# Optimization experiments

Hardware: AMD Instinct MI355X
Metric: run time of the kernel (lower is better)

The kernel has to match this reference:

```python
import jax, jax.numpy as jnp
import numpy as np

# dims
B, S, D, H, DH, M, L, V, BS, NR = 4, 2048, 512, 8, 64, 2048, 6, 32000, 64, 3
NB = S // BS  # 32 blocks


def _block_plan(nb, seed):
    """BigBird block connectivity: 2 global + 3 window + NR random blocks per query block.
    Returns idx [nb, K] int32 and validity mask [nb, K] bool (dedup + edge handling)."""
    rng = np.random.RandomState(seed)
    K = 5 + NR
    idx = np.zeros((nb, K), np.int32)
    msk = np.zeros((nb, K), bool)
    for i in range(nb):
        fixed = {0, nb - 1} | {j for j in (i - 1, i, i + 1) if 0 <= j < nb}
        rest = [j for j in range(nb) if j not in fixed]
        rnd = rng.choice(rest, size=min(NR, len(rest)), replace=False) if rest else []
        sel = sorted(fixed | set(int(r) for r in rnd))
        idx[i, :len(sel)] = sel
        msk[i, :len(sel)] = True
    return jnp.asarray(idx), jnp.asarray(msk)


def _posemb():
    pos = np.arange(S, dtype=np.float32)[:, None]
    div = np.exp(np.arange(0, D, 2, dtype=np.float32) * (-np.log(10000.0) / D))
    pe = np.zeros((S, D), np.float32)
    pe[:, 0::2] = np.sin(pos * div)
    pe[:, 1::2] = np.cos(pos * div)
    return jnp.asarray(pe)


def _ln(x, scale, bias):
    m = jnp.mean(x, axis=-1, keepdims=True)
    v = jnp.mean(jnp.square(x - m), axis=-1, keepdims=True)
    return (x - m) * jax.lax.rsqrt(v + 1e-6) * scale + bias


def _bigbird_attn(x, key_mask, wq, wk, wv, wo, idx, bmask):
    # x: [B,S,D]; idx/bmask: [NB,K]
    q = jnp.einsum('bsd,dhe->bshe', x, wq).reshape(B, NB, BS, H, DH)
    k = jnp.einsum('bsd,dhe->bshe', x, wk).reshape(B, NB, BS, H, DH)
    v = jnp.einsum('bsd,dhe->bshe', x, wv).reshape(B, NB, BS, H, DH)
    kg = k[:, idx]  # [B,NB,K,BS,H,DH] gathered key blocks
    vg = v[:, idx]
    scores = jnp.einsum('bnqhe,bnkche->bhnqkc', q, kg) / jnp.sqrt(jnp.float32(DH))
    kmb = key_mask.reshape(B, NB, BS)[:, idx]          # [B,NB,K,BS]
    m = kmb & bmask[None, :, :, None]                   # [B,NB,K,BS]
    scores = jnp.where(m[:, None, :, None, :, :], scores, jnp.float32(-1e9))
    Kc = idx.shape[1]
    attn = jax.nn.softmax(scores.reshape(B, H, NB, BS, Kc * BS), axis=-1)
    attn = attn.reshape(B, H, NB, BS, Kc, BS)
    out = jnp.einsum('bhnqkc,bnkche->bnqhe', attn, vg).reshape(B, S, H, DH)
    return jnp.einsum('bshe,hed->bsd', out, wo)


def setup_inputs() -> dict:
    key = jax.random.key(0)
    ks = jax.random.split(key, 12)
    n = jax.random.normal
    inp = {
        'tokens': jax.random.randint(ks[0], (B, S), 0, V, dtype=jnp.int32),
        'embed': n(ks[1], (V, D), dtype=jnp.float32),
        'ln1_s': jnp.ones((L, D), jnp.float32), 'ln1_b': jnp.zeros((L, D), jnp.float32),
        'wq': n(ks[2], (L, D, H, DH), dtype=jnp.float32) * 0.02,
        'wk': n(ks[3], (L, D, H, DH), dtype=jnp.float32) * 0.02,
        'wv': n(ks[4], (L, D, H, DH), dtype=jnp.float32) * 0.02,
        'wo': n(ks[5], (L, H, DH, D), dtype=jnp.float32) * 0.02,
        'ln2_s': jnp.ones((L, D), jnp.float32), 'ln2_b': jnp.zeros((L, D), jnp.float32),
        'w1': n(ks[6], (L, D, M), dtype=jnp.float32) * 0.02, 'b1': jnp.zeros((L, M), jnp.float32),
        'w2': n(ks[7], (L, M, D), dtype=jnp.float32) * 0.02, 'b2': jnp.zeros((L, D), jnp.float32),
        'lnf_s': jnp.ones((D,), jnp.float32), 'lnf_b': jnp.zeros((D,), jnp.float32),
    }
    return inp


def reference(tokens, embed, ln1_s, ln1_b, wq, wk, wv, wo, ln2_s, ln2_b, w1, b1, w2, b2, lnf_s, lnf_b):
    key_mask = tokens > 0                      # src padding mask
    x = embed[tokens] + _posemb()[None]        # [B,S,D]
    plans = [_block_plan(NB, l) for l in range(L)]  # connectivity_seed = layer index
    for l in range(L):
        idx, bm = plans[l]
        h = _ln(x, ln1_s[l], ln1_b[l])
        x = x + _bigbird_attn(h, key_mask, wq[l], wk[l], wv[l], wo[l], idx, bm)
        y = _ln(x, ln2_s[l], ln2_b[l])
        y = jax.nn.gelu(jnp.einsum('bsd,dm->bsm', y, w1[l]) + b1[l])
        y = jnp.einsum('bsm,md->bsd', y, w2[l]) + b2[l]
        x = x + y
    return _ln(x, lnf_s, lnf_b)
```

## Files before the change

### kernel.cpp

```cpp
#include <hip/hip_runtime.h>

using u32 = unsigned int;
using u16 = unsigned short;

#define B_   4
#define S_   2048
#define D_   512
#define H_   8
#define DH_  64
#define FF_  2048
#define L_   6
#define NB_  32
#define KC_  8

typedef __attribute__((ext_vector_type(8))) __bf16 bf16x8;
typedef __attribute__((ext_vector_type(4))) float  f32x4;

struct Plan { unsigned char idx[NB_][KC_]; unsigned char cnt[NB_]; };

#define QSCALE 0.18033688011112042f

__device__ __forceinline__ u16 f2b(float f) {
  union { __bf16 b; u16 u; } x;
  x.b = (__bf16)f;
  return x.u;
}

__device__ __forceinline__ float gelu_f(float x) {
  float y2 = 1.5957691216f * x + 0.0713548163f * x * x * x;
  return x / (1.0f + __expf(-y2));
}

typedef const __attribute__((address_space(1))) u32* gas_t;
typedef __attribute__((address_space(3))) u32* las_t;
__device__ __forceinline__ void glds16(const u16* g, u16* l) {
  __builtin_amdgcn_global_load_lds((gas_t)g, (las_t)l, 16, 0, 0);
}

__global__ __launch_bounds__(256)
void transpose_conv(const float* __restrict__ in, u16* __restrict__ out, int R, int C,
                    size_t lstride, int rowoff) {
  __shared__ float tile[32][33];
  const int l = blockIdx.z;
  const float* src = in + (size_t)l * R * C;
  u16* dst = out + (size_t)l * lstride;
  const int c0 = blockIdx.x * 32, r0 = blockIdx.y * 32;
  const int tx = threadIdx.x, ty = threadIdx.y;
#pragma unroll
  for (int i = 0; i < 4; i++)
    tile[ty + i * 8][tx] = src[(size_t)(r0 + ty + i * 8) * C + c0 + tx];
  __syncthreads();
#pragma unroll
  for (int i = 0; i < 4; i++)
    dst[(size_t)(rowoff + c0 + ty + i * 8) * R + r0 + tx] = f2b(tile[tx][ty + i * 8]);
}

__global__ __launch_bounds__(128)
void embed_kernel(const int* __restrict__ tokens, const float* __restrict__ emb,
                  float* __restrict__ x) {
  const int row = blockIdx.x;
  const int s = row & (S_ - 1);
  const int t = threadIdx.x;
  const int tok = tokens[row];
  float4 v = ((const float4*)(emb + (size_t)tok * D_))[t];
  float va[4] = {v.x, v.y, v.z, v.w};
  const float cc = -2.0f * logf(10000.0f) / (float)D_;
  const float pos = (float)s;
#pragma unroll
  for (int j = 0; j < 4; j++) {
    int d = t * 4 + j;
    int i = d >> 1;
    float dv = expf(cc * (float)i);
    float ang = pos * dv;
    va[j] += (d & 1) ? cosf(ang) : sinf(ang);
  }
  ((float4*)x)[(size_t)row * (D_ / 4) + t] = make_float4(va[0], va[1], va[2], va[3]);
}

template <bool BF16OUT>
__global__ __launch_bounds__(128)
void ln_kernel(const float* __restrict__ x, const float* __restrict__ sc,
               const float* __restrict__ bi, void* __restrict__ outp) {
  const int row = blockIdx.x;
  const int t = threadIdx.x;
  float4 v = ((const float4*)(x + (size_t)row * D_))[t];
  float va[4] = {v.x, v.y, v.z, v.w};
  float s = va[0] + va[1] + va[2] + va[3];
  float sq = va[0] * va[0] + va[1] * va[1] + va[2] * va[2] + va[3] * va[3];
#pragma unroll
  for (int d = 1; d < 64; d <<= 1) {
    s  += __shfl_xor(s, d);
    sq += __shfl_xor(sq, d);
  }
  __shared__ float red[4];
  const int wv = t >> 6, lane = t & 63;
  if (lane == 0) { red[wv * 2] = s; red[wv * 2 + 1] = sq; }
  __syncthreads();
  const float ts  = red[0] + red[2];
  const float tsq = red[1] + red[3];
  const float mean = ts * (1.0f / (float)D_);
  const float inv  = rsqrtf(tsq * (1.0f / (float)D_) - mean * mean + 1e-6f);
  const int d0 = t * 4;
  float o[4];
#pragma unroll
  for (int j = 0; j < 4; j++)
    o[j] = (va[j] - mean) * inv * sc[d0 + j] + bi[d0 + j];
  if (BF16OUT) {
    ushort4 u;
    u.x = f2b(o[0]); u.y = f2b(o[1]); u.z = f2b(o[2]); u.w = f2b(o[3]);
    ((ushort4*)outp)[(size_t)row * (D_ / 4) + t] = u;
  } else {
    ((float4*)outp)[(size_t)row * (D_ / 4) + t] = make_float4(o[0], o[1], o[2], o[3]);
  }
}

template <int MODE, bool VSPLIT, int T>
__global__ __launch_bounds__(T * 2)
void gemm_pipe(const u16* __restrict__ A, const u16* __restrict__ BT,
               int Kk, int ostride,
               float* __restrict__ outf, u16* __restrict__ outb,
               const float* __restrict__ bias, const float* __restrict__ resid,
               u16* __restrict__ vtout) {
  constexpr int MI = T / 32;
  constexpr int NW = T / 64;
  __shared__ u16 As[2][T * 64];
  __shared__ u16 Bs[2][T * 64];
  const int tid = threadIdx.x;
  const int wave = tid >> 6, lane = tid & 63;
  const int row0 = blockIdx.x * T, col0 = blockIdx.y * T;
  const int wr = wave / NW, wc = wave % NW;
  const int l15 = lane & 15, l4 = lane >> 4;

  const u16* asrc[4];
  const u16* bsrc[4];
  int cdst[4];
#pragma unroll
  for (int i = 0; i < 4; i++) {
    int chunk = wave * 256 + i * 64 + lane;
    int r = chunk >> 3, s = chunk & 7;
    int ss = (s ^ (r & 7)) << 3;
    asrc[i] = A  + (size_t)(row0 + r) * Kk + ss;
    bsrc[i] = BT + (size_t)(col0 + r) * Kk + ss;
    cdst[i] = (wave * 256 + i * 64) * 8;
  }

  int aoff[MI], boff[4];
#pragma unroll
  for (int m = 0; m < MI; m++) aoff[m] = (wr * (MI * 16) + m * 16 + l15) * 64;
#pragma unroll
  for (int n = 0; n < 4; n++) boff[n] = (wc * 64 + n * 16 + l15) * 64;
  const int sk0 = ((l4)     ^ (l15 & 7)) << 3;
  const int sk1 = ((4 + l4) ^ (l15 & 7)) << 3;

  f32x4 acc[MI][4] = {};
  const int nk = Kk >> 6;

  auto stage = [&](int buf, int kt) {
    const int ko = kt << 6;
#pragma unroll
    for (int i = 0; i < 4; i++) glds16(asrc[i] + ko, &As[buf][cdst[i]]);
#pragma unroll
    for (int i = 0; i < 4; i++) glds16(bsrc[i] + ko, &Bs[buf][cdst[i]]);
  };

  stage(0, 0);
  stage(1, 1);

  for (int kt = 0; kt < nk; ++kt) {
    const int cur = kt & 1;
    if (kt + 1 < nk) { asm volatile("s_waitcnt vmcnt(8)" ::: "memory"); }
    else             { asm volatile("s_waitcnt vmcnt(0)" ::: "memory"); }
    __builtin_amdgcn_s_barrier();
    __builtin_amdgcn_sched_barrier(0);

    bf16x8 af0[MI], bf0[4];
#pragma unroll
    for (int m = 0; m < MI; m++) af0[m] = *(const bf16x8*)&As[cur][aoff[m] + sk0];
#pragma unroll
    for (int n = 0; n < 4; n++) bf0[n] = *(const bf16x8*)&Bs[cur][boff[n] + sk0];
#pragma unroll
    for (int m = 0; m < MI; m++)
#pragma unroll
      for (int n = 0; n < 4; n++)
        acc[m][n] = __builtin_amdgcn_mfma_f32_16x16x32_bf16(af0[m], bf0[n], acc[m][n], 0, 0, 0);

    bf16x8 af1[MI], bf1[4];
#pragma unroll
    for (int m = 0; m < MI; m++) af1[m] = *(const bf16x8*)&As[cur][aoff[m] + sk1];
#pragma unroll
    for (int n = 0; n < 4; n++) bf1[n] = *(const bf16x8*)&Bs[cur][boff[n] + sk1];
    asm volatile("s_waitcnt lgkmcnt(0)" ::: "memory");
    __builtin_amdgcn_sched_barrier(0);
    __builtin_amdgcn_s_barrier();
    __builtin_amdgcn_sched_barrier(0);
    if (kt + 2 < nk) stage(cur, kt + 2);

    __builtin_amdgcn_s_setprio(1);
#pragma unroll
    for (int m = 0; m < MI; m++)
#pragma unroll
      for (int n = 0; n < 4; n++)
        acc[m][n] = __builtin_amdgcn_mfma_f32_16x16x32_bf16(af1[m], bf1[n], acc[m][n], 0, 0, 0);
    __builtin_amdgcn_s_setprio(0);
  }

#pragma unroll
  for (int m = 0; m < MI; m++) {
#pragma unroll
    for (int n = 0; n < 4; n++) {
      const int c = col0 + wc * 64 + n * 16 + l15;
      const int rb = row0 + wr * (MI * 16) + m * 16 + l4 * 4;
      if (VSPLIT && c >= 1024) {
        u16 pk[4];
#pragma unroll
        for (int j = 0; j < 4; j++) pk[j] = f2b(acc[m][n][j]);
        *(uint2*)(vtout + (size_t)(c - 1024) * (B_ * S_) + rb) = *(const uint2*)pk;
      } else {
#pragma unroll
        for (int j = 0; j < 4; j++) {
          const size_t o = (size_t)(rb + j) * ostride + c;
          float v = acc[m][n][j];
          if (MODE == 0) {
            if (VSPLIT && c < 512) v *= QSCALE;
            outb[o] = f2b(v);
          } else if (MODE == 1) {
            outf[o] = v + resid[o];
          } else if (MODE == 2) {
            outb[o] = f2b(gelu_f(v + bias[c]));
          } else {
            outf[o] = v + bias[c] + resid[o];
          }
        }
      }
    }
  }
}

__global__ __launch_bounds__(256, 4)
void attn_mfma(const u16* __restrict__ qkv, const u16* __restrict__ vTg,
               const int* __restrict__ tokens, u16* __restrict__ outb, Plan plan) {
  __shared__ u16 ks[2][64 * 64];
  __shared__ u16 vt[2][64 * 64];
  __shared__ u16 ps[64 * 64];

  const int blk = blockIdx.x;
  const int h0 = blk & 7;
  const int n  = (blk >> 3) & 31;
  const int b  = blk >> 8;
  const int t  = threadIdx.x;
  const int wave = t >> 6, lane = t & 63;
  const int l15 = lane & 15, l4 = lane >> 4;
  const int ncnt = plan.cnt[n];
  const int qrow0 = b * S_ + n * 64;

  auto stage = [&](int bi, int c, int* tkd) {
    const int krow0 = b * S_ + c * 64;
#pragma unroll
    for (int i = 0; i < 2; i++) {
      int c0 = i * 256 + wave * 64;
      int cl = c0 + lane;
      int r = cl >> 3, s = cl & 7;
      int sw = (s ^ (r & 7)) << 3;
      glds16(qkv + (size_t)(krow0 + r) * 1024 + 512 + h0 * 64 + sw, &ks[bi][c0 * 8]);
      glds16(vTg + (size_t)(h0 * 64 + r) * (B_ * S_) + krow0 + sw, &vt[bi][c0 * 8]);
    }
#pragma unroll
    for (int nn = 0; nn < 4; nn++) tkd[nn] = tokens[krow0 + nn * 16 + l15];
  };

  bf16x8 qaf[2];
#pragma unroll
  for (int ks_ = 0; ks_ < 2; ks_++)
    qaf[ks_] = *(const bf16x8*)(qkv + (size_t)(qrow0 + wave * 16 + l15) * 1024 +
                                h0 * 64 + ks_ * 32 + l4 * 8);

  int tk[4], tn[4];
  stage(0, plan.idx[n][0], tk);

  f32x4 oacc[4] = {};
  float mrow[4], lrow[4];
#pragma unroll
  for (int j = 0; j < 4; j++) { mrow[j] = -3e38f; lrow[j] = 0.0f; }

  for (int kc = 0; kc < ncnt; kc++) {
    const int cur = kc & 1;
    __syncthreads();
    if (kc + 1 < ncnt) stage(cur ^ 1, plan.idx[n][kc + 1], tn);

    f32x4 sacc[4] = {};
#pragma unroll
    for (int nn = 0; nn < 4; nn++) {
      int r = nn * 16 + l15;
#pragma unroll
      for (int ks_ = 0; ks_ < 2; ks_++) {
        bf16x8 kf = *(const bf16x8*)(&ks[cur][r * 64 + ((ks_ * 32 + l4 * 8) ^ ((r & 7) << 3))]);
        sacc[nn] = __builtin_amdgcn_mfma_f32_16x16x32_bf16(qaf[ks_], kf, sacc[nn], 0, 0, 0);
      }
    }

    bool vld[4];
#pragma unroll
    for (int nn = 0; nn < 4; nn++) vld[nn] = tk[nn] > 0;

    float rmax[4];
#pragma unroll
    for (int j = 0; j < 4; j++) {
      float mj = -3e38f;
#pragma unroll
      for (int nn = 0; nn < 4; nn++)
        if (vld[nn]) mj = fmaxf(mj, sacc[nn][j]);
      rmax[j] = mj;
    }
#pragma unroll
    for (int d = 1; d < 16; d <<= 1) {
#pragma unroll
      for (int j = 0; j < 4; j++) rmax[j] = fmaxf(rmax[j], __shfl_xor(rmax[j], d));
    }
    int chg = 0;
#pragma unroll
    for (int j = 0; j < 4; j++) chg |= (rmax[j] > mrow[j]);
    if (__ballot(chg)) {
#pragma unroll
      for (int j = 0; j < 4; j++) {
        float mn = fmaxf(mrow[j], rmax[j]);
        float alpha = exp2f(mrow[j] - mn);
        mrow[j] = mn;
        lrow[j] *= alpha;
#pragma unroll
        for (int n2 = 0; n2 < 4; n2++) oacc[n2][j] *= alpha;
      }
    }
    float p[4][4];
#pragma unroll
    for (int j = 0; j < 4; j++) {
      float psum = 0.0f;
#pragma unroll
      for (int nn = 0; nn < 4; nn++) {
        float pv = vld[nn] ? exp2f(sacc[nn][j] - mrow[j]) : 0.0f;
        p[nn][j] = pv;
        psum += pv;
      }
      lrow[j] += psum;
    }

#pragma unroll
    for (int nn = 0; nn < 4; nn++)
#pragma unroll
      for (int j = 0; j < 4; j++) {
        int q = wave * 16 + l4 * 4 + j;
        ps[q * 64 + ((nn * 16 + l15) ^ ((q & 7) << 3))] = f2b(p[nn][j]);
      }

#pragma unroll
    for (int ks_ = 0; ks_ < 2; ks_++) {
      int r = wave * 16 + l15;
      bf16x8 paf = *(const bf16x8*)(ps + r * 64 + ((ks_ * 32 + l4 * 8) ^ ((r & 7) << 3)));
#pragma unroll
      for (int n2 = 0; n2 < 4; n2++) {
        int rv = n2 * 16 + l15;
        bf16x8 vf = *(const bf16x8*)(&vt[cur][rv * 64 + ((ks_ * 32 + l4 * 8) ^ ((rv & 7) << 3))]);
        oacc[n2] = __builtin_amdgcn_mfma_f32_16x16x32_bf16(paf, vf, oacc[n2], 0, 0, 0);
      }
    }
#pragma unroll
    for (int nn = 0; nn < 4; nn++) tk[nn] = tn[nn];
  }

#pragma unroll
  for (int d = 1; d < 16; d <<= 1) {
#pragma unroll
    for (int j = 0; j < 4; j++) lrow[j] += __shfl_xor(lrow[j], d);
  }
#pragma unroll
  for (int j = 0; j < 4; j++) {
    const float inv = lrow[j] > 0.0f ? 1.0f / lrow[j] : 0.0f;
    const int q = n * 64 + wave * 16 + l4 * 4 + j;
#pragma unroll
    for (int n2 = 0; n2 < 4; n2++) {
      outb[(size_t)(b * S_ + q) * D_ + h0 * 64 + n2 * 16 + l15] = f2b(oacc[n2][j] * inv);
    }
  }
}

namespace {
struct HostMT {
  u32 mt[624]; int mti;
  void seed(u32 s) {
    mt[0] = s;
    for (int i = 1; i < 624; i++)
      mt[i] = 1812433253u * (mt[i - 1] ^ (mt[i - 1] >> 30)) + (u32)i;
    mti = 624;
  }
  u32 next() {
    if (mti >= 624) {
      for (int k = 0; k < 624; k++) {
        u32 y = (mt[k] & 0x80000000u) | (mt[(k + 1) % 624] & 0x7fffffffu);
        mt[k] = mt[(k + 397) % 624] ^ (y >> 1) ^ ((y & 1u) ? 0x9908b0dfu : 0u);
      }
      mti = 0;
    }
    u32 y = mt[mti++];
    y ^= y >> 11;
    y ^= (y << 7)  & 0x9d2c5680u;
    y ^= (y << 15) & 0xefc60000u;
    y ^= y >> 18;
    return y;
  }
  u32 interval(u32 mx) {
    if (mx == 0u) return 0u;
    u32 mask = mx;
    mask |= mask >> 1; mask |= mask >> 2; mask |= mask >> 4;
    mask |= mask >> 8; mask |= mask >> 16;
    u32 v;
    while ((v = (next() & mask)) > mx) {}
    return v;
  }
};

void build_plan(int l, Plan* out) {
  HostMT rng;
  rng.seed((u32)l);
  for (int i = 0; i < NB_; i++) {
    bool fixedv[NB_] = {};
    fixedv[0] = true; fixedv[NB_ - 1] = true;
    for (int j = i - 1; j <= i + 1; j++)
      if (j >= 0 && j < NB_) fixedv[j] = true;
    int rest[NB_]; int nr = 0;
    for (int j = 0; j < NB_; j++) if (!fixedv[j]) rest[nr++] = j;
    int perm[NB_];
    for (int tt = 0; tt < nr; tt++) perm[tt] = tt;
    for (int tt = nr - 1; tt >= 1; tt--) {
      int j = (int)rng.interval((u32)tt);
      int tmp = perm[tt]; perm[tt] = perm[j]; perm[j] = tmp;
    }
    bool sel[NB_];
    for (int j = 0; j < NB_; j++) sel[j] = fixedv[j];
    for (int c = 0; c < 3; c++) sel[rest[perm[c]]] = true;
    int cnt = 0;
    for (int j = 0; j < NB_; j++)
      if (sel[j]) out->idx[i][cnt++] = (unsigned char)j;
    out->cnt[i] = (unsigned char)cnt;
    for (int c2 = cnt; c2 < KC_; c2++) out->idx[i][c2] = 0;
  }
}
}

extern "C" void kernel_launch(void* const* d_in, const int* in_sizes, int n_in,
                              void* d_out, int out_size, void* d_ws, size_t ws_size,
                              hipStream_t stream) {
  (void)in_sizes; (void)n_in; (void)out_size; (void)ws_size;

  const int*   tokens = (const int*)d_in[0];
  const float* embed  = (const float*)d_in[1];
  const float* ln1_s  = (const float*)d_in[2];
  const float* ln1_b  = (const float*)d_in[3];
  const float* wq     = (const float*)d_in[4];
  const float* wk     = (const float*)d_in[5];
  const float* wv     = (const float*)d_in[6];
  const float* wo     = (const float*)d_in[7];
  const float* ln2_s  = (const float*)d_in[8];
  const float* ln2_b  = (const float*)d_in[9];
  const float* w1     = (const float*)d_in[10];
  const float* b1     = (const float*)d_in[11];
  const float* w2     = (const float*)d_in[12];
  const float* b2     = (const float*)d_in[13];
  const float* lnf_s  = (const float*)d_in[14];
  const float* lnf_b  = (const float*)d_in[15];

  char* wp = (char*)d_ws;
  auto take = [&](size_t bytes) {
    void* p = (void*)wp;
    wp += (bytes + 255) & ~(size_t)255;
    return p;
  };

  const int Mrows = B_ * S_;
  u16* wqkvT = (u16*)take((size_t)L_ * 1536 * D_ * 2);
  u16* woT   = (u16*)take((size_t)L_ * D_ * D_ * 2);
  u16* w1T   = (u16*)take((size_t)L_ * FF_ * D_ * 2);
  u16* w2T   = (u16*)take((size_t)L_ * D_ * FF_ * 2);
  float* x   = (float*)take((size_t)Mrows * D_ * 4);
  u16* h     = (u16*)take((size_t)Mrows * D_ * 2);
  u16* big   = (u16*)take((size_t)Mrows * FF_ * 2);
  u16* qkv   = big;
  u16* vT    = big + (size_t)Mrows * 1024;
  u16* g     = big;

  Plan plans[L_];
  for (int l = 0; l < L_; l++) build_plan(l, &plans[l]);

  const size_t qkvL = (size_t)1536 * D_;

  transpose_conv<<<dim3(D_ / 32, D_ / 32, L_), dim3(32, 8), 0, stream>>>(wq, wqkvT, D_, D_, qkvL, 0);
  transpose_conv<<<dim3(D_ / 32, D_ / 32, L_), dim3(32, 8), 0, stream>>>(wk, wqkvT, D_, D_, qkvL, 512);
  transpose_conv<<<dim3(D_ / 32, D_ / 32, L_), dim3(32, 8), 0, stream>>>(wv, wqkvT, D_, D_, qkvL, 1024);
  transpose_conv<<<dim3(D_ / 32, D_ / 32, L_), dim3(32, 8), 0, stream>>>(wo, woT, D_, D_, (size_t)D_ * D_, 0);
  transpose_conv<<<dim3(FF_ / 32, D_ / 32, L_), dim3(32, 8), 0, stream>>>(w1, w1T, D_, FF_, (size_t)FF_ * D_, 0);
  transpose_conv<<<dim3(D_ / 32, FF_ / 32, L_), dim3(32, 8), 0, stream>>>(w2, w2T, FF_, D_, (size_t)D_ * FF_, 0);
  embed_kernel<<<Mrows, 128, 0, stream>>>(tokens, embed, x);

  for (int l = 0; l < L_; l++) {
    ln_kernel<true><<<Mrows, 128, 0, stream>>>(x, ln1_s + l * D_, ln1_b + l * D_, h);
    gemm_pipe<0, true, 256><<<dim3(Mrows / 256, 6), 512, 0, stream>>>(
        h, wqkvT + (size_t)l * qkvL, D_, 1024, nullptr, qkv, nullptr, nullptr, vT);
    attn_mfma<<<B_ * NB_ * H_, 256, 0, stream>>>(qkv, vT, tokens, h, plans[l]);
    gemm_pipe<1, false, 128><<<dim3(Mrows / 128, 4), 256, 0, stream>>>(
        h, woT + (size_t)l * D_ * D_, D_, D_, x, nullptr, nullptr, x, nullptr);
    ln_kernel<true><<<Mrows, 128, 0, stream>>>(x, ln2_s + l * D_, ln2_b + l * D_, h);
    gemm_pipe<2, false, 256><<<dim3(Mrows / 256, 8), 512, 0, stream>>>(
        h, w1T + (size_t)l * FF_ * D_, D_, FF_, nullptr, g, b1 + l * FF_, nullptr, nullptr);
    gemm_pipe<3, false, 128><<<dim3(Mrows / 128, 4), 256, 0, stream>>>(
        g, w2T + (size_t)l * D_ * FF_, FF_, D_, x, nullptr, b2 + l * D_, x, nullptr);
  }
  ln_kernel<false><<<Mrows, 128, 0, stream>>>(x, lnf_s, lnf_b, d_out);
}
```

Measured before the change: 878.2 us.

## Use rectangular GEMM tiles with XCD-aware block remapping and smaller tiles

```diff
diff --git a/kernel.cpp b/kernel.cpp
--- a/kernel.cpp
+++ b/kernel.cpp
@@ -114,34 +114,46 @@
   }
 }
 
-template <int MODE, bool VSPLIT, int T>
-__global__ __launch_bounds__(T * 2)
+template <int MODE, bool VSPLIT, int TM, int TN>
+__global__ __launch_bounds__(TN * 2)
 void gemm_pipe(const u16* __restrict__ A, const u16* __restrict__ BT,
-               int Kk, int ostride,
+               int Kk, int ostride, int ncols,
                float* __restrict__ outf, u16* __restrict__ outb,
                const float* __restrict__ bias, const float* __restrict__ resid,
                u16* __restrict__ vtout) {
-  constexpr int MI = T / 32;
-  constexpr int NW = T / 64;
-  __shared__ u16 As[2][T * 64];
-  __shared__ u16 Bs[2][T * 64];
+  constexpr int NW  = TN / 32;
+  constexpr int WC  = NW / 2;
+  constexpr int MI  = TM / 32;
+  constexpr int CHA = TM / (8 * NW);
+  constexpr int CHB = TN / (8 * NW);
+  constexpr int VM  = CHA + CHB;
+  __shared__ u16 As[2][TM * 64];
+  __shared__ u16 Bs[2][TN * 64];
   const int tid = threadIdx.x;
   const int wave = tid >> 6, lane = tid & 63;
-  const int row0 = blockIdx.x * T, col0 = blockIdx.y * T;
-  const int wr = wave / NW, wc = wave % NW;
+  const int nwg = gridDim.x, cpx = nwg >> 3;
+  const int bid = blockIdx.x;
+  const int gid = (bid & 7) * cpx + (bid >> 3);
+  const int row0 = (gid / ncols) * TM, col0 = (gid % ncols) * TN;
+  const int wr = wave / WC, wc = wave % WC;
   const int l15 = lane & 15, l4 = lane >> 4;
 
-  const u16* asrc[4];
-  const u16* bsrc[4];
-  int cdst[4];
-#pragma unroll
-  for (int i = 0; i < 4; i++) {
-    int chunk = wave * 256 + i * 64 + lane;
+  const u16* asrc[CHA];
+  const u16* bsrc[CHB];
+  int adst[CHA], bdst[CHB];
+#pragma unroll
+  for (int i = 0; i < CHA; i++) {
+    int chunk = wave * (CHA * 64) + i * 64 + lane;
     int r = chunk >> 3, s = chunk & 7;
-    int ss = (s ^ (r & 7)) << 3;
-    asrc[i] = A  + (size_t)(row0 + r) * Kk + ss;
-    bsrc[i] = BT + (size_t)(col0 + r) * Kk + ss;
-    cdst[i] = (wave * 256 + i * 64) * 8;
+    asrc[i] = A + (size_t)(row0 + r) * Kk + ((s ^ (r & 7)) << 3);
+    adst[i] = (wave * (CHA * 64) + i * 64) * 8;
+  }
+#pragma unroll
+  for (int i = 0; i < CHB; i++) {
+    int chunk = wave * (CHB * 64) + i * 64 + lane;
+    int r = chunk >> 3, s = chunk & 7;
+    bsrc[i] = BT + (size_t)(col0 + r) * Kk + ((s ^ (r & 7)) << 3);
+    bdst[i] = (wave * (CHB * 64) + i * 64) * 8;
   }
 
   int aoff[MI], boff[4];
@@ -158,9 +170,9 @@
   auto stage = [&](int buf, int kt) {
     const int ko = kt << 6;
 #pragma unroll
-    for (int i = 0; i < 4; i++) glds16(asrc[i] + ko, &As[buf][cdst[i]]);
-#pragma unroll
-    for (int i = 0; i < 4; i++) glds16(bsrc[i] + ko, &Bs[buf][cdst[i]]);
+    for (int i = 0; i < CHA; i++) glds16(asrc[i] + ko, &As[buf][adst[i]]);
+#pragma unroll
+    for (int i = 0; i < CHB; i++) glds16(bsrc[i] + ko, &Bs[buf][bdst[i]]);
   };
 
   stage(0, 0);
@@ -168,8 +180,12 @@
 
   for (int kt = 0; kt < nk; ++kt) {
     const int cur = kt & 1;
-    if (kt + 1 < nk) { asm volatile("s_waitcnt vmcnt(8)" ::: "memory"); }
-    else             { asm volatile("s_waitcnt vmcnt(0)" ::: "memory"); }
+    if (kt + 1 < nk) {
+      if constexpr (VM == 8) { asm volatile("s_waitcnt vmcnt(8)" ::: "memory"); }
+      else                   { asm volatile("s_waitcnt vmcnt(6)" ::: "memory"); }
+    } else {
+      asm volatile("s_waitcnt vmcnt(0)" ::: "memory");
+    }
     __builtin_amdgcn_s_barrier();
     __builtin_amdgcn_sched_barrier(0);
 
@@ -501,16 +517,16 @@
 
   for (int l = 0; l < L_; l++) {
     ln_kernel<true><<<Mrows, 128, 0, stream>>>(x, ln1_s + l * D_, ln1_b + l * D_, h);
-    gemm_pipe<0, true, 256><<<dim3(Mrows / 256, 6), 512, 0, stream>>>(
-        h, wqkvT + (size_t)l * qkvL, D_, 1024, nullptr, qkv, nullptr, nullptr, vT);
+    gemm_pipe<0, true, 128, 128><<<768, 256, 0, stream>>>(
+        h, wqkvT + (size_t)l * qkvL, D_, 1024, 12, nullptr, qkv, nullptr, nullptr, vT);
     attn_mfma<<<B_ * NB_ * H_, 256, 0, stream>>>(qkv, vT, tokens, h, plans[l]);
-    gemm_pipe<1, false, 128><<<dim3(Mrows / 128, 4), 256, 0, stream>>>(
-        h, woT + (size_t)l * D_ * D_, D_, D_, x, nullptr, nullptr, x, nullptr);
+    gemm_pipe<1, false, 64, 128><<<512, 256, 0, stream>>>(
+        h, woT + (size_t)l * D_ * D_, D_, D_, 4, x, nullptr, nullptr, x, nullptr);
     ln_kernel<true><<<Mrows, 128, 0, stream>>>(x, ln2_s + l * D_, ln2_b + l * D_, h);
-    gemm_pipe<2, false, 256><<<dim3(Mrows / 256, 8), 512, 0, stream>>>(
-        h, w1T + (size_t)l * FF_ * D_, D_, FF_, nullptr, g, b1 + l * FF_, nullptr, nullptr);
-    gemm_pipe<3, false, 128><<<dim3(Mrows / 128, 4), 256, 0, stream>>>(
-        g, w2T + (size_t)l * D_ * FF_, FF_, D_, x, nullptr, b2 + l * D_, x, nullptr);
+    gemm_pipe<2, false, 128, 128><<<1024, 256, 0, stream>>>(
+        h, w1T + (size_t)l * FF_ * D_, D_, FF_, 16, nullptr, g, b1 + l * FF_, nullptr, nullptr);
+    gemm_pipe<3, false, 64, 128><<<512, 256, 0, stream>>>(
+        g, w2T + (size_t)l * D_ * FF_, FF_, D_, 4, x, nullptr, b2 + l * D_, x, nullptr);
   }
   ln_kernel<false><<<Mrows, 128, 0, stream>>>(x, lnf_s, lnf_b, d_out);
 }
```

Result: no change. 868.8 us (-1.1%).
